# Kernel tuning notes

Measured on AMD Instinct MI355X. Metric: run time of the kernel, lower is better.

## Reference

```python
import jax, jax.numpy as jnp
import numpy as np

VOCAB, EMB, HID, OUT = 50000, 256, 512, 18
SEQ, BATCH, PAD_IDX = 256, 64, 1


def setup_inputs() -> dict:
    key = jax.random.key(0)
    ks = jax.random.split(key, 16)
    s = 0.05
    emb_table = jax.random.normal(ks[0], (VOCAB, EMB), jnp.float32) * s
    emb_table = emb_table.at[PAD_IDX].set(0.0)  # padding_idx row is zero
    inp = {
        "text": jax.random.randint(ks[1], (SEQ, BATCH), 0, VOCAB),
        "emb_table": emb_table,
        "emfc_w": jax.random.normal(ks[2], (EMB, EMB), jnp.float32) * s,
        "emfc_b": jax.random.normal(ks[3], (EMB,), jnp.float32) * s,
        # layer 0: input size EMB; layer 1: input size 2*HID (bidirectional)
        "w_ih0": jax.random.normal(ks[4], (2, HID, EMB), jnp.float32) * s,
        "w_hh0": jax.random.normal(ks[5], (2, HID, HID), jnp.float32) * s,
        "b_ih0": jax.random.normal(ks[6], (2, HID), jnp.float32) * s,
        "b_hh0": jax.random.normal(ks[7], (2, HID), jnp.float32) * s,
        "w_ih1": jax.random.normal(ks[8], (2, HID, 2 * HID), jnp.float32) * s,
        "w_hh1": jax.random.normal(ks[9], (2, HID, HID), jnp.float32) * s,
        "b_ih1": jax.random.normal(ks[10], (2, HID), jnp.float32) * s,
        "b_hh1": jax.random.normal(ks[11], (2, HID), jnp.float32) * s,
        "fc_w": jax.random.normal(ks[12], (OUT, 2 * HID), jnp.float32) * s,
        "fc_b": jax.random.normal(ks[13], (OUT,), jnp.float32) * s,
    }
    return inp


def _rnn_dir(x, w_ih, w_hh, b_ih, b_hh):
    # x: [S,B,D] -> [S,B,H]; h_t = relu(x W_ih^T + b_ih + h W_hh^T + b_hh)
    xp = jnp.einsum('sbd,hd->sbh', x, w_ih) + (b_ih + b_hh)
    h0 = jnp.zeros((x.shape[1], w_hh.shape[0]), x.dtype)
    def step(h, xt):
        h = jax.nn.relu(xt + h @ w_hh.T)
        return h, h
    _, ys = jax.lax.scan(step, h0, xp)
    return ys


def _bi_rnn_layer(x, w_ih, w_hh, b_ih, b_hh):
    fwd = _rnn_dir(x, w_ih[0], w_hh[0], b_ih[0], b_hh[0])
    bwd = _rnn_dir(x[::-1], w_ih[1], w_hh[1], b_ih[1], b_hh[1])[::-1]
    return jnp.concatenate([fwd, bwd], axis=-1)  # [S,B,2H]


def reference(text, emb_table, emfc_w, emfc_b, w_ih0, w_hh0, b_ih0, b_hh0,
              w_ih1, w_hh1, b_ih1, b_hh1, fc_w, fc_b):
    embedded = emb_table[text]                    # [S,B,EMB] (dropout p=0 -> identity)
    post_emb = embedded @ emfc_w.T + emfc_b       # [S,B,EMB]
    h = _bi_rnn_layer(post_emb, w_ih0, w_hh0, b_ih0, b_hh0)  # [S,B,2H]
    h = _bi_rnn_layer(h, w_ih1, w_hh1, b_ih1, b_hh1)          # [S,B,2H]
    return h @ fc_w.T + fc_b                      # [S,B,OUT]
```

## Files before the change

kernel.cpp:

```cpp
#include <hip/hip_runtime.h>

typedef _Float16 half_t;
typedef _Float16 half4 __attribute__((ext_vector_type(4)));
typedef _Float16 half8 __attribute__((ext_vector_type(8)));
typedef float floatx4 __attribute__((ext_vector_type(4)));
typedef unsigned long long ull_t;

#define SEQ 256
#define BATCH 64
#define EMB 256
#define HID 512
#define NOUT 18
#define M_TOT (SEQ*BATCH)

#define KK_REG 12
#define K_REG  (KK_REG*32)
#define KTAIL  (HID - K_REG)
#define WROW   136
#define HROW   520
#define WLDS_BYTES (HID*WROW*2)
#define HLDS_BYTES (16*HROW*2)
#define LDS_BYTES  (WLDS_BYTES + HLDS_BYTES)

#define O_WHH0_16 0u
#define O_WHH1_16 1048576u
#define O_EMFC16  2097152u
#define O_WIH0    2228224u
#define O_WIH1    2752512u
#define O_FC16    4849664u
#define O_PE      4886528u
#define O_XP      13275136u
#define O_OUT     46829568u

__global__ void cvt_f32f16(const float* __restrict__ s, half_t* __restrict__ d, int n8) {
    int i = blockIdx.x * 256 + threadIdx.x;
    if (i < n8) {
        const float4* s4 = (const float4*)s;
        float4 a = s4[2*i], b = s4[2*i+1];
        half8 h;
        h[0]=(_Float16)a.x; h[1]=(_Float16)a.y; h[2]=(_Float16)a.z; h[3]=(_Float16)a.w;
        h[4]=(_Float16)b.x; h[5]=(_Float16)b.y; h[6]=(_Float16)b.z; h[7]=(_Float16)b.w;
        *(half8*)(d + (size_t)i*8) = h;
    }
}

template<bool GATHER>
__global__ __launch_bounds__(256)
void gemm_nt(const half_t* __restrict__ A, const float* __restrict__ Atab,
             const int* __restrict__ gidx, const half_t* __restrict__ Bm,
             const float* __restrict__ bias0, const float* __restrict__ bias1,
             half_t* __restrict__ Cout, int M, int N, int K)
{
    __shared__ half8 As8[512];
    __shared__ half8 Bs8[512];
    half_t* As = (half_t*)As8;
    half_t* Bs = (half_t*)Bs8;

    const int tid  = threadIdx.x;
    const int lane = tid & 63, wid = tid >> 6;
    const int wm = wid >> 1, wn = wid & 1;
    const int ln = lane & 15, hi = lane >> 4;
    const int m0 = blockIdx.x * 128, n0 = blockIdx.y * 128;

    floatx4 acc[4][4] = {};
    const int kTiles = K >> 5;

    for (int kt = 0; kt < kTiles; ++kt) {
        if constexpr (GATHER) {
            int r = tid >> 1, q = tid & 1;
            int row = gidx[m0 + r];
            const float* src = Atab + (size_t)row * EMB + kt*32 + q*16;
            float4 f0 = *(const float4*)(src);
            float4 f1 = *(const float4*)(src + 4);
            float4 f2 = *(const float4*)(src + 8);
            float4 f3 = *(const float4*)(src + 12);
            half8 h0, h1;
            h0[0]=(_Float16)f0.x; h0[1]=(_Float16)f0.y; h0[2]=(_Float16)f0.z; h0[3]=(_Float16)f0.w;
            h0[4]=(_Float16)f1.x; h0[5]=(_Float16)f1.y; h0[6]=(_Float16)f1.z; h0[7]=(_Float16)f1.w;
            h1[0]=(_Float16)f2.x; h1[1]=(_Float16)f2.y; h1[2]=(_Float16)f2.z; h1[3]=(_Float16)f2.w;
            h1[4]=(_Float16)f3.x; h1[5]=(_Float16)f3.y; h1[6]=(_Float16)f3.z; h1[7]=(_Float16)f3.w;
            int c0 = 2*q, c1 = 2*q + 1;
            *(half8*)(As + r*32 + (((c0 + (r>>1)) & 3) * 8)) = h0;
            *(half8*)(As + r*32 + (((c1 + (r>>1)) & 3) * 8)) = h1;
        } else {
            #pragma unroll
            for (int ii = 0; ii < 2; ++ii) {
                int ch = tid + ii*256; int r = ch >> 2, c = ch & 3;
                half8 v = *(const half8*)(A + (size_t)(m0+r)*K + kt*32 + c*8);
                *(half8*)(As + r*32 + (((c + (r>>1)) & 3) * 8)) = v;
            }
        }
        #pragma unroll
        for (int ii = 0; ii < 2; ++ii) {
            int ch = tid + ii*256; int r = ch >> 2, c = ch & 3;
            half8 v = *(const half8*)(Bm + (size_t)(n0+r)*K + kt*32 + c*8);
            *(half8*)(Bs + r*32 + (((c + (r>>1)) & 3) * 8)) = v;
        }
        __syncthreads();

        half8 af[4], bf[4];
        #pragma unroll
        for (int mt = 0; mt < 4; ++mt) {
            int r = wm*64 + mt*16 + ln;
            af[mt] = *(const half8*)(As + r*32 + ((hi + (r>>1)) & 3) * 8);
        }
        #pragma unroll
        for (int nt = 0; nt < 4; ++nt) {
            int r = wn*64 + nt*16 + ln;
            bf[nt] = *(const half8*)(Bs + r*32 + ((hi + (r>>1)) & 3) * 8);
        }
        #pragma unroll
        for (int mt = 0; mt < 4; ++mt)
            #pragma unroll
            for (int nt = 0; nt < 4; ++nt)
                acc[mt][nt] = __builtin_amdgcn_mfma_f32_16x16x32_f16(af[mt], bf[nt], acc[mt][nt], 0, 0, 0);
        __syncthreads();
    }

    #pragma unroll
    for (int mt = 0; mt < 4; ++mt) {
        #pragma unroll
        for (int nt = 0; nt < 4; ++nt) {
            int n = n0 + wn*64 + nt*16 + ln;
            float bv = (bias0 ? bias0[n] : 0.f) + (bias1 ? bias1[n] : 0.f);
            #pragma unroll
            for (int r = 0; r < 4; ++r) {
                int m = m0 + wm*64 + mt*16 + hi*4 + r;
                Cout[(size_t)m*N + n] = (half_t)(acc[mt][nt][r] + bv);
            }
        }
    }
}

__global__ __launch_bounds__(512, 2)
void rnn_layer(const half_t* __restrict__ xp, half_t* __restrict__ outbuf,
               const half_t* __restrict__ whh16)
{
    extern __shared__ char smem[];
    half_t* wlds = (half_t*)smem;
    half_t* hlds = (half_t*)(smem + WLDS_BYTES);

    const int bid = blockIdx.x;
    const int dir = bid >> 2;
    const int bg  = bid & 3;
    const int w   = threadIdx.x >> 6;
    const int lane = threadIdx.x & 63;
    const int ln = lane & 15, hi = lane >> 4;

    const half_t* wbase = whh16 + (size_t)dir * HID * HID;

    half8 afrag[4][KK_REG];
    #pragma unroll
    for (int mt = 0; mt < 4; ++mt) {
        #pragma unroll
        for (int kk = 0; kk < KK_REG; ++kk)
            afrag[mt][kk] = *(const half8*)(wbase + (size_t)(w*64 + mt*16 + ln)*HID + kk*32 + hi*8);
    }

    for (int idx = threadIdx.x; idx < HID*16; idx += 512) {
        int row = idx >> 4, c8 = idx & 15;
        *(half8*)(wlds + row*WROW + c8*8) =
            *(const half8*)(wbase + (size_t)row*HID + K_REG + c8*8);
    }

    const int b  = bg*16 + ln;
    const int jq = w*64 + hi*4;

    const ptrdiff_t dstep = dir ? -(ptrdiff_t)(BATCH*2*HID) : (ptrdiff_t)(BATCH*2*HID);
    const int t0 = dir ? (SEQ-1) : 0;
    const size_t base0 = ((size_t)(t0*BATCH + b))*(2*HID) + (size_t)dir*HID + jq;
    const half_t* xb = xp + base0;
    half_t*       op = outbuf + base0;

    const half_t* hrd = hlds + (size_t)ln*HROW + hi*8;
    half_t*       hwr = hlds + (size_t)ln*HROW + jq;
    const half_t* wrd = wlds + (size_t)(w*64 + ln)*WROW + hi*8;

    half4 xq[4];
    #pragma unroll
    for (int mt = 0; mt < 4; ++mt) xq[mt] = *(const half4*)(xb + mt*16);
    xb += dstep;

    floatx4 acc[4];
    #pragma unroll
    for (int mt = 0; mt < 4; ++mt) {
        acc[mt][0] = (float)xq[mt][0]; acc[mt][1] = (float)xq[mt][1];
        acc[mt][2] = (float)xq[mt][2]; acc[mt][3] = (float)xq[mt][3];
    }
    #pragma unroll
    for (int mt = 0; mt < 4; ++mt) xq[mt] = *(const half4*)(xb + mt*16);
    xb += dstep;

    {
        half4 hv[4];
        #pragma unroll
        for (int mt = 0; mt < 4; ++mt) {
            #pragma unroll
            for (int r = 0; r < 4; ++r)
                hv[mt][r] = (_Float16)fmaxf(acc[mt][r], 0.f);
            *(half4*)(hwr + mt*16) = hv[mt];
            *(half4*)(op  + mt*16) = hv[mt];
        }
        op += dstep;
    }
    asm volatile("s_waitcnt lgkmcnt(0)\n\ts_barrier" ::: "memory");

    for (int step = 1; step < SEQ; ++step) {
        #pragma unroll
        for (int mt = 0; mt < 4; ++mt) {
            acc[mt][0] = (float)xq[mt][0]; acc[mt][1] = (float)xq[mt][1];
            acc[mt][2] = (float)xq[mt][2]; acc[mt][3] = (float)xq[mt][3];
        }
        if (step + 1 < SEQ) {
            #pragma unroll
            for (int mt = 0; mt < 4; ++mt) xq[mt] = *(const half4*)(xb + mt*16);
        }
        xb += dstep;

        __builtin_amdgcn_s_setprio(1);
        half8 c0 = *(const half8*)(hrd + 0*32);
        half8 c1 = *(const half8*)(hrd + 1*32);
        #pragma unroll
        for (int g = 0; g < 5; ++g) {
            half8 n0 = *(const half8*)(hrd + (2*g+2)*32);
            half8 n1 = *(const half8*)(hrd + (2*g+3)*32);
            #pragma unroll
            for (int mt = 0; mt < 4; ++mt)
                acc[mt] = __builtin_amdgcn_mfma_f32_16x16x32_f16(afrag[mt][2*g],   c0, acc[mt], 0, 0, 0);
            #pragma unroll
            for (int mt = 0; mt < 4; ++mt)
                acc[mt] = __builtin_amdgcn_mfma_f32_16x16x32_f16(afrag[mt][2*g+1], c1, acc[mt], 0, 0, 0);
            c0 = n0; c1 = n1;
        }
        #pragma unroll
        for (int mt = 0; mt < 4; ++mt)
            acc[mt] = __builtin_amdgcn_mfma_f32_16x16x32_f16(afrag[mt][10], c0, acc[mt], 0, 0, 0);
        #pragma unroll
        for (int mt = 0; mt < 4; ++mt)
            acc[mt] = __builtin_amdgcn_mfma_f32_16x16x32_f16(afrag[mt][11], c1, acc[mt], 0, 0, 0);

        #pragma unroll
        for (int kt = 0; kt < 4; ++kt) {
            half8 ch = *(const half8*)(hrd + K_REG + kt*32);
            half8 w0 = *(const half8*)(wrd + 0*16*WROW + kt*32);
            half8 w1 = *(const half8*)(wrd + 1*16*WROW + kt*32);
            half8 w2 = *(const half8*)(wrd + 2*16*WROW + kt*32);
            half8 w3 = *(const half8*)(wrd + 3*16*WROW + kt*32);
            acc[0] = __builtin_amdgcn_mfma_f32_16x16x32_f16(w0, ch, acc[0], 0, 0, 0);
            acc[1] = __builtin_amdgcn_mfma_f32_16x16x32_f16(w1, ch, acc[1], 0, 0, 0);
            acc[2] = __builtin_amdgcn_mfma_f32_16x16x32_f16(w2, ch, acc[2], 0, 0, 0);
            acc[3] = __builtin_amdgcn_mfma_f32_16x16x32_f16(w3, ch, acc[3], 0, 0, 0);
        }
        __builtin_amdgcn_s_setprio(0);

        half4 hv[4];
        #pragma unroll
        for (int mt = 0; mt < 4; ++mt) {
            #pragma unroll
            for (int r = 0; r < 4; ++r)
                hv[mt][r] = (_Float16)fmaxf(acc[mt][r], 0.f);
        }

        if (step + 1 < SEQ) {
            asm volatile("s_waitcnt lgkmcnt(0)\n\ts_barrier" ::: "memory");
            #pragma unroll
            for (int mt = 0; mt < 4; ++mt)
                *(half4*)(hwr + mt*16) = hv[mt];
            asm volatile("s_waitcnt lgkmcnt(0)\n\ts_barrier" ::: "memory");
        }

        #pragma unroll
        for (int mt = 0; mt < 4; ++mt)
            *(half4*)(op + mt*16) = hv[mt];
        op += dstep;
    }
}

__global__ __launch_bounds__(256)
void fc_kernel(const half_t* __restrict__ X, const half_t* __restrict__ W16,
               const float* __restrict__ bias, float* __restrict__ Y)
{
    __shared__ half8 Ws8[2304];
    half_t* Ws = (half_t*)Ws8;
    for (int ch = threadIdx.x; ch < 2304; ch += 256)
        Ws8[ch] = *(const half8*)(W16 + (size_t)ch*8);
    __syncthreads();

    int wi = threadIdx.x >> 6, lane = threadIdx.x & 63;
    int m = blockIdx.x*4 + wi;
    const half_t* xr = X + (size_t)m*1024 + lane*16;
    half8 x0 = *(const half8*)xr;
    half8 x1 = *(const half8*)(xr + 8);
    float xa[16];
    #pragma unroll
    for (int i = 0; i < 8; ++i) { xa[i] = (float)x0[i]; xa[8+i] = (float)x1[i]; }

    for (int n = 0; n < NOUT; ++n) {
        const half_t* wr = Ws + n*1024 + lane*16;
        half8 w0 = *(const half8*)wr;
        half8 w1 = *(const half8*)(wr + 8);
        float s = 0.f;
        #pragma unroll
        for (int i = 0; i < 8; ++i) s += xa[i]*(float)w0[i] + xa[8+i]*(float)w1[i];
        #pragma unroll
        for (int off = 32; off > 0; off >>= 1) s += __shfl_down(s, off, 64);
        if (lane == 0) Y[(size_t)m*NOUT + n] = s + bias[n];
    }
}

extern "C" void kernel_launch(void* const* d_in, const int* in_sizes, int n_in,
                              void* d_out, int out_size, void* d_ws, size_t ws_size,
                              hipStream_t stream)
{
    const int*   text    = (const int*)  d_in[0];
    const float* emb     = (const float*)d_in[1];
    const float* emfc_w  = (const float*)d_in[2];
    const float* emfc_b  = (const float*)d_in[3];
    const float* w_ih0   = (const float*)d_in[4];
    const float* w_hh0   = (const float*)d_in[5];
    const float* b_ih0   = (const float*)d_in[6];
    const float* b_hh0   = (const float*)d_in[7];
    const float* w_ih1   = (const float*)d_in[8];
    const float* w_hh1   = (const float*)d_in[9];
    const float* b_ih1   = (const float*)d_in[10];
    const float* b_hh1   = (const float*)d_in[11];
    const float* fc_w    = (const float*)d_in[12];
    const float* fc_b    = (const float*)d_in[13];
    float* out = (float*)d_out;

    char* ws = (char*)d_ws;
    half_t* whh0_16 = (half_t*)(ws + O_WHH0_16);
    half_t* whh1_16 = (half_t*)(ws + O_WHH1_16);
    half_t* emfc16  = (half_t*)(ws + O_EMFC16);
    half_t* wih0    = (half_t*)(ws + O_WIH0);
    half_t* wih1    = (half_t*)(ws + O_WIH1);
    half_t* fc16    = (half_t*)(ws + O_FC16);
    half_t* pe      = (half_t*)(ws + O_PE);
    half_t* xp      = (half_t*)(ws + O_XP);
    half_t* out0    = (half_t*)(ws + O_OUT);
    half_t* out1    = (half_t*)(ws + O_OUT);

    static int attr_done = 0;
    if (!attr_done) {
        hipFuncSetAttribute((const void*)rnn_layer,
                            hipFuncAttributeMaxDynamicSharedMemorySize, LDS_BYTES);
        attr_done = 1;
    }

    cvt_f32f16<<<32,  256, 0, stream>>>(emfc_w, emfc16, 8192);
    cvt_f32f16<<<128, 256, 0, stream>>>(w_ih0,  wih0,  32768);
    cvt_f32f16<<<512, 256, 0, stream>>>(w_ih1,  wih1, 131072);
    cvt_f32f16<<<256, 256, 0, stream>>>(w_hh0,  whh0_16, 65536);
    cvt_f32f16<<<256, 256, 0, stream>>>(w_hh1,  whh1_16, 65536);
    cvt_f32f16<<<9,   256, 0, stream>>>(fc_w,   fc16,   2304);

    gemm_nt<true><<<dim3(M_TOT/128, EMB/128), 256, 0, stream>>>(
        nullptr, emb, text, emfc16, emfc_b, nullptr, pe, M_TOT, EMB, EMB);

    gemm_nt<false><<<dim3(M_TOT/128, (2*HID)/128), 256, 0, stream>>>(
        pe, nullptr, nullptr, wih0, b_ih0, b_hh0, xp, M_TOT, 2*HID, EMB);

    rnn_layer<<<8, 512, LDS_BYTES, stream>>>(xp, out0, whh0_16);

    gemm_nt<false><<<dim3(M_TOT/128, (2*HID)/128), 256, 0, stream>>>(
        out0, nullptr, nullptr, wih1, b_ih1, b_hh1, xp, M_TOT, 2*HID, 2*HID);

    rnn_layer<<<8, 512, LDS_BYTES, stream>>>(xp, out1, whh1_16);

    fc_kernel<<<M_TOT/4, 256, 0, stream>>>(out1, fc16, fc_b, out);
}
```

Measured before the change: 1.427 ms.

## Hold full W_hh in registers and double-buffer hidden state to drop a barrier

Each wave now keeps all 16 K-slices of its recurrent weight fragments in registers, instead of keeping 12 and streaming the last 128 columns from LDS every step. This removes the LDS weight tile and the per-step LDS weight reads. The hidden-state buffer in LDS is double-buffered, so each step needs one barrier instead of two before and after writing h. The cost is much higher register pressure (256 registers of weight fragments per thread), which risks spills or lower occupancy in this latency-bound recurrent loop.

```diff
diff --git a/kernel.cpp b/kernel.cpp
--- a/kernel.cpp
+++ b/kernel.cpp
@@ -13,14 +13,7 @@
 #define NOUT 18
 #define M_TOT (SEQ*BATCH)
 
-#define KK_REG 12
-#define K_REG  (KK_REG*32)
-#define KTAIL  (HID - K_REG)
-#define WROW   136
-#define HROW   520
-#define WLDS_BYTES (HID*WROW*2)
-#define HLDS_BYTES (16*HROW*2)
-#define LDS_BYTES  (WLDS_BYTES + HLDS_BYTES)
+#define HROW 520
 
 #define O_WHH0_16 0u
 #define O_WHH1_16 1048576u
@@ -136,9 +129,7 @@
 void rnn_layer(const half_t* __restrict__ xp, half_t* __restrict__ outbuf,
                const half_t* __restrict__ whh16)
 {
-    extern __shared__ char smem[];
-    half_t* wlds = (half_t*)smem;
-    half_t* hlds = (half_t*)(smem + WLDS_BYTES);
+    __shared__ half_t hlds[2][16][HROW];
 
     const int bid = blockIdx.x;
     const int dir = bid >> 2;
@@ -149,18 +140,12 @@
 
     const half_t* wbase = whh16 + (size_t)dir * HID * HID;
 
-    half8 afrag[4][KK_REG];
+    half8 afrag[4][16];
     #pragma unroll
     for (int mt = 0; mt < 4; ++mt) {
         #pragma unroll
-        for (int kk = 0; kk < KK_REG; ++kk)
+        for (int kk = 0; kk < 16; ++kk)
             afrag[mt][kk] = *(const half8*)(wbase + (size_t)(w*64 + mt*16 + ln)*HID + kk*32 + hi*8);
-    }
-
-    for (int idx = threadIdx.x; idx < HID*16; idx += 512) {
-        int row = idx >> 4, c8 = idx & 15;
-        *(half8*)(wlds + row*WROW + c8*8) =
-            *(const half8*)(wbase + (size_t)row*HID + K_REG + c8*8);
     }
 
     const int b  = bg*16 + ln;
@@ -172,9 +157,8 @@
     const half_t* xb = xp + base0;
     half_t*       op = outbuf + base0;
 
-    const half_t* hrd = hlds + (size_t)ln*HROW + hi*8;
-    half_t*       hwr = hlds + (size_t)ln*HROW + jq;
-    const half_t* wrd = wlds + (size_t)(w*64 + ln)*WROW + hi*8;
+    const half_t* hrd0 = &hlds[0][ln][hi*8];
+    half_t*       hwr0 = &hlds[0][ln][jq];
 
     half4 xq[4];
     #pragma unroll
@@ -198,7 +182,7 @@
             #pragma unroll
             for (int r = 0; r < 4; ++r)
                 hv[mt][r] = (_Float16)fmaxf(acc[mt][r], 0.f);
-            *(half4*)(hwr + mt*16) = hv[mt];
+            *(half4*)(hwr0 + mt*16) = hv[mt];
             *(half4*)(op  + mt*16) = hv[mt];
         }
         op += dstep;
@@ -206,6 +190,10 @@
     asm volatile("s_waitcnt lgkmcnt(0)\n\ts_barrier" ::: "memory");
 
     for (int step = 1; step < SEQ; ++step) {
+        const int rb = (step + 1) & 1;
+        const int wb = step & 1;
+        const half_t* hrd = hrd0 + (size_t)rb*16*HROW;
+
         #pragma unroll
         for (int mt = 0; mt < 4; ++mt) {
             acc[mt][0] = (float)xq[mt][0]; acc[mt][1] = (float)xq[mt][1];
@@ -221,7 +209,7 @@
         half8 c0 = *(const half8*)(hrd + 0*32);
         half8 c1 = *(const half8*)(hrd + 1*32);
         #pragma unroll
-        for (int g = 0; g < 5; ++g) {
+        for (int g = 0; g < 7; ++g) {
             half8 n0 = *(const half8*)(hrd + (2*g+2)*32);
             half8 n1 = *(const half8*)(hrd + (2*g+3)*32);
             #pragma unroll
@@ -234,23 +222,10 @@
         }
         #pragma unroll
         for (int mt = 0; mt < 4; ++mt)
-            acc[mt] = __builtin_amdgcn_mfma_f32_16x16x32_f16(afrag[mt][10], c0, acc[mt], 0, 0, 0);
+            acc[mt] = __builtin_amdgcn_mfma_f32_16x16x32_f16(afrag[mt][14], c0, acc[mt], 0, 0, 0);
         #pragma unroll
         for (int mt = 0; mt < 4; ++mt)
-            acc[mt] = __builtin_amdgcn_mfma_f32_16x16x32_f16(afrag[mt][11], c1, acc[mt], 0, 0, 0);
-
-        #pragma unroll
-        for (int kt = 0; kt < 4; ++kt) {
-            half8 ch = *(const half8*)(hrd + K_REG + kt*32);
-            half8 w0 = *(const half8*)(wrd + 0*16*WROW + kt*32);
-            half8 w1 = *(const half8*)(wrd + 1*16*WROW + kt*32);
-            half8 w2 = *(const half8*)(wrd + 2*16*WROW + kt*32);
-            half8 w3 = *(const half8*)(wrd + 3*16*WROW + kt*32);
-            acc[0] = __builtin_amdgcn_mfma_f32_16x16x32_f16(w0, ch, acc[0], 0, 0, 0);
-            acc[1] = __builtin_amdgcn_mfma_f32_16x16x32_f16(w1, ch, acc[1], 0, 0, 0);
-            acc[2] = __builtin_amdgcn_mfma_f32_16x16x32_f16(w2, ch, acc[2], 0, 0, 0);
-            acc[3] = __builtin_amdgcn_mfma_f32_16x16x32_f16(w3, ch, acc[3], 0, 0, 0);
-        }
+            acc[mt] = __builtin_amdgcn_mfma_f32_16x16x32_f16(afrag[mt][15], c1, acc[mt], 0, 0, 0);
         __builtin_amdgcn_s_setprio(0);
 
         half4 hv[4];
@@ -262,10 +237,10 @@
         }
 
         if (step + 1 < SEQ) {
-            asm volatile("s_waitcnt lgkmcnt(0)\n\ts_barrier" ::: "memory");
+            half_t* hw = hwr0 + (size_t)wb*16*HROW;
             #pragma unroll
             for (int mt = 0; mt < 4; ++mt)
-                *(half4*)(hwr + mt*16) = hv[mt];
+                *(half4*)(hw + mt*16) = hv[mt];
             asm volatile("s_waitcnt lgkmcnt(0)\n\ts_barrier" ::: "memory");
         }
 
@@ -340,13 +315,6 @@
     half_t* out0    = (half_t*)(ws + O_OUT);
     half_t* out1    = (half_t*)(ws + O_OUT);
 
-    static int attr_done = 0;
-    if (!attr_done) {
-        hipFuncSetAttribute((const void*)rnn_layer,
-                            hipFuncAttributeMaxDynamicSharedMemorySize, LDS_BYTES);
-        attr_done = 1;
-    }
-
     cvt_f32f16<<<32,  256, 0, stream>>>(emfc_w, emfc16, 8192);
     cvt_f32f16<<<128, 256, 0, stream>>>(w_ih0,  wih0,  32768);
     cvt_f32f16<<<512, 256, 0, stream>>>(w_ih1,  wih1, 131072);
@@ -360,12 +328,12 @@
     gemm_nt<false><<<dim3(M_TOT/128, (2*HID)/128), 256, 0, stream>>>(
         pe, nullptr, nullptr, wih0, b_ih0, b_hh0, xp, M_TOT, 2*HID, EMB);
 
-    rnn_layer<<<8, 512, LDS_BYTES, stream>>>(xp, out0, whh0_16);
+    rnn_layer<<<8, 512, 0, stream>>>(xp, out0, whh0_16);
 
     gemm_nt<false><<<dim3(M_TOT/128, (2*HID)/128), 256, 0, stream>>>(
         out0, nullptr, nullptr, wih1, b_ih1, b_hh1, xp, M_TOT, 2*HID, 2*HID);
 
-    rnn_layer<<<8, 512, LDS_BYTES, stream>>>(xp, out1, whh1_16);
+    rnn_layer<<<8, 512, 0, stream>>>(xp, out1, whh1_16);
 
     fc_kernel<<<M_TOT/4, 256, 0, stream>>>(out1, fc16, fc_b, out);
 }
```

New measurement: 2.629 ms. 84.1% more time.

## Double-buffer RNN hidden state in LDS and XOR-swizzle LDS layouts

Applied to the files above, without the earlier changes.

Switches the LDS hidden-state buffer to two ping-pong buffers so each step can write the new h without first waiting on a barrier for all reads to finish. This drops one of the two per-step workgroup barriers. It also replaces the padded row strides with an XOR swizzle on both the weight tail tile and the hidden buffer to avoid bank conflicts. The cost is extra LDS (two 16KB h buffers) and more address arithmetic.

```diff
diff --git a/kernel.cpp b/kernel.cpp
--- a/kernel.cpp
+++ b/kernel.cpp
@@ -15,12 +15,9 @@
 
 #define KK_REG 12
 #define K_REG  (KK_REG*32)
-#define KTAIL  (HID - K_REG)
-#define WROW   136
-#define HROW   520
-#define WLDS_BYTES (HID*WROW*2)
-#define HLDS_BYTES (16*HROW*2)
-#define LDS_BYTES  (WLDS_BYTES + HLDS_BYTES)
+#define WTILE_BYTES (HID*256)
+#define HBUF_BYTES  (16*1024)
+#define LDS_BYTES (WTILE_BYTES + 2*HBUF_BYTES)
 
 #define O_WHH0_16 0u
 #define O_WHH1_16 1048576u
@@ -137,8 +134,8 @@
                const half_t* __restrict__ whh16)
 {
     extern __shared__ char smem[];
-    half_t* wlds = (half_t*)smem;
-    half_t* hlds = (half_t*)(smem + WLDS_BYTES);
+    char* wlds = smem;
+    char* hlds = smem + WTILE_BYTES;
 
     const int bid = blockIdx.x;
     const int dir = bid >> 2;
@@ -146,6 +143,7 @@
     const int w   = threadIdx.x >> 6;
     const int lane = threadIdx.x & 63;
     const int ln = lane & 15, hi = lane >> 4;
+    const int sw = (ln & 7) << 4;
 
     const half_t* wbase = whh16 + (size_t)dir * HID * HID;
 
@@ -159,7 +157,7 @@
 
     for (int idx = threadIdx.x; idx < HID*16; idx += 512) {
         int row = idx >> 4, c8 = idx & 15;
-        *(half8*)(wlds + row*WROW + c8*8) =
+        *(half8*)(wlds + row*256 + ((c8*16) ^ ((row & 7) << 4))) =
             *(const half8*)(wbase + (size_t)row*HID + K_REG + c8*8);
     }
 
@@ -172,9 +170,8 @@
     const half_t* xb = xp + base0;
     half_t*       op = outbuf + base0;
 
-    const half_t* hrd = hlds + (size_t)ln*HROW + hi*8;
-    half_t*       hwr = hlds + (size_t)ln*HROW + jq;
-    const half_t* wrd = wlds + (size_t)(w*64 + ln)*WROW + hi*8;
+    char* hrow = hlds + ln*1024;
+    char* wrow = wlds + (w*64 + ln)*256;
 
     half4 xq[4];
     #pragma unroll
@@ -198,14 +195,18 @@
             #pragma unroll
             for (int r = 0; r < 4; ++r)
                 hv[mt][r] = (_Float16)fmaxf(acc[mt][r], 0.f);
-            *(half4*)(hwr + mt*16) = hv[mt];
-            *(half4*)(op  + mt*16) = hv[mt];
+            *(half4*)(hrow + ((w*128 + hi*8 + mt*32) ^ sw)) = hv[mt];
+            *(half4*)(op + mt*16) = hv[mt];
         }
         op += dstep;
     }
     asm volatile("s_waitcnt lgkmcnt(0)\n\ts_barrier" ::: "memory");
 
     for (int step = 1; step < SEQ; ++step) {
+        const int rb = (step + 1) & 1;
+        const int wb = step & 1;
+        const char* hrd = hrow + rb*HBUF_BYTES;
+
         #pragma unroll
         for (int mt = 0; mt < 4; ++mt) {
             acc[mt][0] = (float)xq[mt][0]; acc[mt][1] = (float)xq[mt][1];
@@ -218,12 +219,12 @@
         xb += dstep;
 
         __builtin_amdgcn_s_setprio(1);
-        half8 c0 = *(const half8*)(hrd + 0*32);
-        half8 c1 = *(const half8*)(hrd + 1*32);
+        half8 c0 = *(const half8*)(hrd + ((0*64 + hi*16) ^ sw));
+        half8 c1 = *(const half8*)(hrd + ((1*64 + hi*16) ^ sw));
         #pragma unroll
         for (int g = 0; g < 5; ++g) {
-            half8 n0 = *(const half8*)(hrd + (2*g+2)*32);
-            half8 n1 = *(const half8*)(hrd + (2*g+3)*32);
+            half8 n0 = *(const half8*)(hrd + (((2*g+2)*64 + hi*16) ^ sw));
+            half8 n1 = *(const half8*)(hrd + (((2*g+3)*64 + hi*16) ^ sw));
             #pragma unroll
             for (int mt = 0; mt < 4; ++mt)
                 acc[mt] = __builtin_amdgcn_mfma_f32_16x16x32_f16(afrag[mt][2*g],   c0, acc[mt], 0, 0, 0);
@@ -241,11 +242,11 @@
 
         #pragma unroll
         for (int kt = 0; kt < 4; ++kt) {
-            half8 ch = *(const half8*)(hrd + K_REG + kt*32);
-            half8 w0 = *(const half8*)(wrd + 0*16*WROW + kt*32);
-            half8 w1 = *(const half8*)(wrd + 1*16*WROW + kt*32);
-            half8 w2 = *(const half8*)(wrd + 2*16*WROW + kt*32);
-            half8 w3 = *(const half8*)(wrd + 3*16*WROW + kt*32);
+            half8 ch = *(const half8*)(hrd + (((KK_REG+kt)*64 + hi*16) ^ sw));
+            half8 w0 = *(const half8*)(wrow + 0*16*256 + ((kt*64 + hi*16) ^ sw));
+            half8 w1 = *(const half8*)(wrow + 1*16*256 + ((kt*64 + hi*16) ^ sw));
+            half8 w2 = *(const half8*)(wrow + 2*16*256 + ((kt*64 + hi*16) ^ sw));
+            half8 w3 = *(const half8*)(wrow + 3*16*256 + ((kt*64 + hi*16) ^ sw));
             acc[0] = __builtin_amdgcn_mfma_f32_16x16x32_f16(w0, ch, acc[0], 0, 0, 0);
             acc[1] = __builtin_amdgcn_mfma_f32_16x16x32_f16(w1, ch, acc[1], 0, 0, 0);
             acc[2] = __builtin_amdgcn_mfma_f32_16x16x32_f16(w2, ch, acc[2], 0, 0, 0);
@@ -262,10 +263,10 @@
         }
 
         if (step + 1 < SEQ) {
-            asm volatile("s_waitcnt lgkmcnt(0)\n\ts_barrier" ::: "memory");
+            char* hw = hrow + wb*HBUF_BYTES;
             #pragma unroll
             for (int mt = 0; mt < 4; ++mt)
-                *(half4*)(hwr + mt*16) = hv[mt];
+                *(half4*)(hw + ((w*128 + hi*8 + mt*32) ^ sw)) = hv[mt];
             asm volatile("s_waitcnt lgkmcnt(0)\n\ts_barrier" ::: "memory");
         }
 
```

Measured after the change: 2.180 ms. 52.7% more time.
